# Kernel optimization log

Hardware: AMD Instinct MI355X
Metric: run time of the kernel (lower is better)

## Reference

```python
import jax, jax.numpy as jnp
import numpy as np

SCALE_FACTORS = (1, 2, 4)
N, T, F = 4096, 128, 128
MARKET = 64
MIX = sum(T // k for k in SCALE_FACTORS)  # 224


def hardswish(x):
    return x * jnp.clip(x + 3.0, 0.0, 6.0) * (1.0 / 6.0)


def layernorm2d(x, g, b, eps=1e-5):
    # LayerNorm with normalized_shape == last two dims (as in torch nn.LayerNorm((A, B)))
    mu = jnp.mean(x, axis=(-2, -1), keepdims=True)
    var = jnp.var(x, axis=(-2, -1), keepdims=True)
    return (x - mu) * jax.lax.rsqrt(var + eps) * g + b


def setup_inputs() -> dict:
    key = jax.random.key(0)
    ks = jax.random.split(key, 32)
    inp = {"x": jax.random.normal(ks[0], (N, T, F), jnp.float32)}
    i = 1
    for si, k in enumerate(SCALE_FACTORS):
        tk = T // k
        inp[f"cw{si}"] = jax.random.normal(ks[i], (F, F, k), jnp.float32) * 0.05; i += 1
        inp[f"cb{si}"] = jnp.zeros((F,), jnp.float32)
        inp[f"lg{si}"] = jnp.ones((tk, F), jnp.float32)
        inp[f"lb{si}"] = jnp.zeros((tk, F), jnp.float32)
        inp[f"L1_{si}"] = jax.random.normal(ks[i], (tk, tk), jnp.float32) * 0.01; i += 1
        inp[f"L2_{si}"] = jax.random.normal(ks[i], (tk, tk), jnp.float32) * 0.01; i += 1
    inp["fc_w"] = jax.random.normal(ks[i], (1, F), jnp.float32) * 0.05; i += 1
    inp["fc_b"] = jnp.zeros((1,), jnp.float32)
    inp["sm_lg"] = jnp.ones((N, MIX), jnp.float32)
    inp["sm_lb"] = jnp.zeros((N, MIX), jnp.float32)
    inp["M1"] = jax.random.normal(ks[i], (MARKET, N), jnp.float32); i += 1
    inp["M2"] = jax.random.normal(ks[i], (N, MARKET), jnp.float32); i += 1
    inp["sm_fc_w"] = jax.random.normal(ks[i], (1, 2 * MIX), jnp.float32) * 0.02; i += 1
    inp["sm_fc_b"] = jnp.zeros((1,), jnp.float32)
    return inp


def _forward(x, cw0, cb0, lg0, lb0, L1_0, L2_0,
             cw1, cb1, lg1, lb1, L1_1, L2_1,
             cw2, cb2, lg2, lb2, L1_2, L2_2,
             fc_w, fc_b, sm_lg, sm_lb, M1, M2, sm_fc_w, sm_fc_b):
    n, t, f = x.shape
    per_scale = ((cw0, cb0, lg0, lb0, L1_0, L2_0),
                 (cw1, cb1, lg1, lb1, L1_1, L2_1),
                 (cw2, cb2, lg2, lb2, L1_2, L2_2))
    parts = []
    for k, (cw, cb, lg, lb, L1, L2) in zip(SCALE_FACTORS, per_scale):
        tk = t // k
        # Conv1d(kernel=k, stride=k) == blockwise contraction over non-overlapping windows
        xr = x.transpose(0, 2, 1).reshape(n, f, tk, k)          # (n, F_in, tk, k)
        xt = jnp.einsum('nitk,oik->nto', xr, cw) + cb            # (n, tk, F)
        # TimeMixing: ragged prefix loop == single lower-triangular matmul over time
        mask = jnp.tril(jnp.ones((tk, tk), x.dtype))
        h = layernorm2d(xt, lg, lb)
        u = hardswish(jnp.einsum('ts,nsf->ntf', L1 * mask, h))
        v = jnp.einsum('ts,nsf->ntf', L2 * mask, u)
        xt = xt + v
        parts.append(xt @ fc_w[0] + fc_b[0])                     # (n, tk)
    h = jnp.concatenate(parts, axis=1)                           # (n, MIX)
    # StockMixing
    hn = layernorm2d(h, sm_lg, sm_lb)
    z = M2 @ hardswish(M1 @ hn)                                  # (n, MIX)
    out = jnp.concatenate([h, h + z], axis=1)                    # (n, 2*MIX)
    return out @ sm_fc_w[0][:, None] + sm_fc_b                   # (n, 1)


def reference(x, cw0, cb0, lg0, lb0, L1_0, L2_0,
              cw1, cb1, lg1, lb1, L1_1, L2_1,
              cw2, cb2, lg2, lb2, L1_2, L2_2,
              fc_w, fc_b, sm_lg, sm_lb, M1, M2, sm_fc_w, sm_fc_b):
    return _forward(x, cw0, cb0, lg0, lb0, L1_0, L2_0,
                    cw1, cb1, lg1, lb1, L1_1, L2_1,
                    cw2, cb2, lg2, lb2, L1_2, L2_2,
                    fc_w, fc_b, sm_lg, sm_lb, M1, M2, sm_fc_w, sm_fc_b)
```

## Files before the change

kernel.cpp:

```cpp
#include <hip/hip_runtime.h>
#include <stdint.h>

typedef __attribute__((ext_vector_type(8))) short short8;
typedef __attribute__((ext_vector_type(4))) float f32x4;
typedef __attribute__((ext_vector_type(4))) unsigned short us4;

__device__ __forceinline__ unsigned short f2bf(float f) {
  union { float f; unsigned int i; } v; v.f = f;
  return (unsigned short)((v.i + 0x7FFFu + ((v.i >> 16) & 1u)) >> 16);
}
__device__ __forceinline__ float hswish(float x) {
  float t = fminf(fmaxf(x + 3.f, 0.f), 6.f);
  return x * t * (1.f / 6.f);
}
__device__ __forceinline__ short8 ldcvt8(const float* __restrict__ p) {
  float4 v0 = *(const float4*)p;
  float4 v1 = *(const float4*)(p + 4);
  short8 r;
  r[0] = (short)f2bf(v0.x); r[1] = (short)f2bf(v0.y);
  r[2] = (short)f2bf(v0.z); r[3] = (short)f2bf(v0.w);
  r[4] = (short)f2bf(v1.x); r[5] = (short)f2bf(v1.y);
  r[6] = (short)f2bf(v1.z); r[7] = (short)f2bf(v1.w);
  return r;
}

__global__ void prep_kernel(const float* __restrict__ cw0, const float* __restrict__ cw1,
                            const float* __restrict__ cw2,
                            const float* __restrict__ L1_0, const float* __restrict__ L2_0,
                            const float* __restrict__ L1_1, const float* __restrict__ L2_1,
                            const float* __restrict__ L1_2, const float* __restrict__ L2_2,
                            unsigned short* __restrict__ ws16) {
  int idx = blockIdx.x * 256 + threadIdx.x;
  if (idx < 16384) {
    ws16[idx] = f2bf(cw0[idx]);
  } else if (idx < 49152) {
    int t = idx - 16384; int o = t >> 8, m = t & 255, j = m >> 7, i = m & 127;
    ws16[idx] = f2bf(cw1[(o * 128 + i) * 2 + j]);
  } else if (idx < 114688) {
    int t = idx - 49152; int o = t >> 9, m = t & 511, j = m >> 7, i = m & 127;
    ws16[idx] = f2bf(cw2[(o * 128 + i) * 4 + j]);
  } else if (idx < 212992) {
    int u = idx - 114688; int which = u >> 14; int e = u & 16383;
    int t = e >> 7, s = e & 127;
    float val = 0.f;
    if (which == 0)      { if (s <= t) val = L1_0[t * 128 + s]; }
    else if (which == 1) { if (s <= t) val = L2_0[t * 128 + s]; }
    else if (which == 2) { if ((s >> 6) == (t >> 6) && (s & 63) <= (t & 63)) val = L1_1[(t & 63) * 64 + (s & 63)]; }
    else if (which == 3) { if ((s >> 6) == (t >> 6) && (s & 63) <= (t & 63)) val = L2_1[(t & 63) * 64 + (s & 63)]; }
    else if (which == 4) { if ((s >> 5) == (t >> 5) && (s & 31) <= (t & 31)) val = L1_2[(t & 31) * 32 + (s & 31)]; }
    else                 { if ((s >> 5) == (t >> 5) && (s & 31) <= (t & 31)) val = L2_2[(t & 31) * 32 + (s & 31)]; }
    ws16[idx] = f2bf(val);
  }
}

__global__ void xcvt_kernel(const float* __restrict__ x, unsigned short* __restrict__ xbf) {
  const float4* x4 = (const float4*)x;
  us4* o4 = (us4*)xbf;
#pragma unroll
  for (int j = 0; j < 4; ++j) {
    int idx = blockIdx.x * 1024 + j * 256 + threadIdx.x;
    float4 v = x4[idx];
    us4 p; p[0] = f2bf(v.x); p[1] = f2bf(v.y); p[2] = f2bf(v.z); p[3] = f2bf(v.w);
    o4[idx] = p;
  }
}

template <bool XBF>
__device__ __forceinline__ short8 load_a(const float* __restrict__ xf,
                                         const unsigned short* __restrict__ xb, int off) {
  if constexpr (XBF) return *(const short8*)&xb[off];
  else return ldcvt8(xf + off);
}

template <int S, bool XBF>
__launch_bounds__(256, 3)
__global__ void s1_tile(const float* __restrict__ xf, const unsigned short* __restrict__ xb,
                        const float* __restrict__ cb, const float* __restrict__ lg,
                        const float* __restrict__ lb,
                        const float* __restrict__ fc_w, const float* __restrict__ fc_b,
                        const unsigned short* __restrict__ cwLT,
                        const unsigned short* __restrict__ L1blk,
                        const unsigned short* __restrict__ L2blk,
                        float* __restrict__ h_out) {
  constexpr int K = 128 << S;
  constexpr int LOG2TK = 7 - S;
  constexpr int TKM = (128 >> S) - 1;
  constexpr int SAMPLES = 1 << S;
  constexpr int OFF = (S == 0) ? 0 : (S == 1 ? 128 : 192);
  constexpr int NK = K / 32;
  constexpr int GSH = 3 - S;
  constexpr float INVD = 1.f / (float)((TKM + 1) * 128);

  __shared__ unsigned short HT[128 * 128];
  __shared__ float scr[272];
  float* part = scr + 128;

  const int tid = threadIdx.x, wave = tid >> 6, lane = tid & 63;
  const int quad = lane >> 4, l16 = lane & 15;
  const int Tb = (wave & 1) * 4, Ob = (wave >> 1) * 4;
  const int n0 = blockIdx.x << S;
  const int abase = n0 * 16384;
  const float fcb = fc_b[0];

  if (tid < 128) { scr[tid] = fc_w[tid]; part[tid] = 0.f; }
  else if (tid < 144) scr[tid + 128] = 0.f;
  __syncthreads();

  f32x4 acc[4][4];
#pragma unroll
  for (int tt = 0; tt < 4; ++tt)
#pragma unroll
    for (int oo = 0; oo < 4; ++oo) acc[tt][oo] = (f32x4){0.f, 0.f, 0.f, 0.f};
#pragma unroll
  for (int ks = 0; ks < NK; ++ks) {
    short8 a[4];
#pragma unroll
    for (int tt = 0; tt < 4; ++tt)
      a[tt] = load_a<XBF>(xf, xb, abase + ((Tb + tt) * 16 + l16) * K + ks * 32 + quad * 8);
#pragma unroll
    for (int oo = 0; oo < 4; ++oo) {
      short8 b = *(const short8*)&cwLT[((Ob + oo) * 16 + l16) * K + ks * 32 + quad * 8];
#pragma unroll
      for (int tt = 0; tt < 4; ++tt)
        acc[tt][oo] = __builtin_amdgcn_mfma_f32_16x16x32_bf16(a[tt], b, acc[tt][oo], 0, 0, 0);
    }
  }

  float ts[4] = {0.f, 0.f, 0.f, 0.f}, tq[4] = {0.f, 0.f, 0.f, 0.f};
#pragma unroll
  for (int oo = 0; oo < 4; ++oo) {
    float cbv = cb[(Ob + oo) * 16 + l16];
#pragma unroll
    for (int tt = 0; tt < 4; ++tt)
#pragma unroll
      for (int r = 0; r < 4; ++r) {
        float v = acc[tt][oo][r] + cbv;
        acc[tt][oo][r] = v;
        ts[tt] += v; tq[tt] += v * v;
      }
  }
  {
    constexpr int GPW = (S == 2) ? 2 : 1;
    float gs[2] = {0.f, 0.f}, gq[2] = {0.f, 0.f};
#pragma unroll
    for (int tt = 0; tt < 4; ++tt) {
      int gl = (S == 2) ? (tt >> 1) : 0;
      gs[gl] += ts[tt]; gq[gl] += tq[tt];
    }
#pragma unroll
    for (int j = 0; j < GPW; ++j) {
      float s = gs[j], q = gq[j];
#pragma unroll
      for (int m = 32; m >= 1; m >>= 1) { s += __shfl_xor(s, m); q += __shfl_xor(q, m); }
      if (lane == 0) {
        int g = (Tb >> GSH) + j;
        atomicAdd(&scr[256 + 2 * g], s);
        atomicAdd(&scr[257 + 2 * g], q);
      }
    }
  }
  __syncthreads();
  if (tid < SAMPLES) {
    float mu = scr[256 + 2 * tid] * INVD;
    float var = scr[257 + 2 * tid] * INVD - mu * mu;
    scr[264 + tid] = mu; scr[268 + tid] = rsqrtf(var + 1e-5f);
  }
  __syncthreads();

#pragma unroll
  for (int tt = 0; tt < 4; ++tt)
#pragma unroll
    for (int r = 0; r < 4; ++r) {
      float v = 0.f;
#pragma unroll
      for (int oo = 0; oo < 4; ++oo) v += acc[tt][oo][r] * scr[(Ob + oo) * 16 + l16];
      v += __shfl_xor(v, 1); v += __shfl_xor(v, 2);
      v += __shfl_xor(v, 4); v += __shfl_xor(v, 8);
      if (l16 == 0) atomicAdd(&part[(Tb + tt) * 16 + quad * 4 + r], v);
    }

#pragma unroll
  for (int tt = 0; tt < 4; ++tt) {
    int tile = Tb + tt, g = tile >> GSH;
    float mu = scr[264 + g], rs = scr[268 + g];
    int tlb = (tile * 16) & TKM;
#pragma unroll
    for (int oo = 0; oo < 4; ++oo) {
      int f = (Ob + oo) * 16 + l16;
      int kf = (f ^ (f >> 3)) & 15;
#pragma unroll
      for (int r = 0; r < 4; ++r) {
        int t = tile * 16 + quad * 4 + r;
        int tl = tlb + quad * 4 + r;
        float hv = (acc[tt][oo][r] - mu) * rs * lg[tl * 128 + f] + lb[tl * 128 + f];
        HT[f * 128 + ((((t >> 3) ^ kf) << 3) | (t & 7))] = f2bf(hv);
      }
    }
  }
  __syncthreads();

  f32x4 u[4][4];
#pragma unroll
  for (int tt = 0; tt < 4; ++tt)
#pragma unroll
    for (int oo = 0; oo < 4; ++oo) u[tt][oo] = (f32x4){0.f, 0.f, 0.f, 0.f};
#pragma unroll
  for (int ks = 0; ks < 4; ++ks) {
    short8 a[4]; bool act[4]; bool any = false;
#pragma unroll
    for (int tt = 0; tt < 4; ++tt) {
      int tile = Tb + tt, g = tile >> GSH;
      act[tt] = (ks * 32 <= tile * 16 + 15) && (ks * 32 + 31 >= (g << LOG2TK));
      if (act[tt]) { a[tt] = *(const short8*)&L1blk[(tile * 16 + l16) * 128 + ks * 32 + quad * 8]; any = true; }
    }
    if (!any) continue;
#pragma unroll
    for (int oo = 0; oo < 4; ++oo) {
      int f = (Ob + oo) * 16 + l16;
      int kf = (f ^ (f >> 3)) & 15;
      short8 b = *(const short8*)&HT[f * 128 + (((ks * 4 + quad) ^ kf) << 3)];
#pragma unroll
      for (int tt = 0; tt < 4; ++tt)
        if (act[tt]) u[tt][oo] = __builtin_amdgcn_mfma_f32_16x16x32_bf16(a[tt], b, u[tt][oo], 0, 0, 0);
    }
  }
  __syncthreads();

#pragma unroll
  for (int tt = 0; tt < 4; ++tt) {
    int tile = Tb + tt;
#pragma unroll
    for (int oo = 0; oo < 4; ++oo) {
      int f = (Ob + oo) * 16 + l16;
      int kf = (f ^ (f >> 3)) & 15;
#pragma unroll
      for (int r = 0; r < 4; ++r) {
        int t = tile * 16 + quad * 4 + r;
        HT[f * 128 + ((((t >> 3) ^ kf) << 3) | (t & 7))] = f2bf(hswish(u[tt][oo][r]));
      }
    }
  }
  __syncthreads();

#pragma unroll
  for (int tt = 0; tt < 4; ++tt)
#pragma unroll
    for (int oo = 0; oo < 4; ++oo) u[tt][oo] = (f32x4){0.f, 0.f, 0.f, 0.f};
#pragma unroll
  for (int ks = 0; ks < 4; ++ks) {
    short8 a[4]; bool act[4]; bool any = false;
#pragma unroll
    for (int tt = 0; tt < 4; ++tt) {
      int tile = Tb + tt, g = tile >> GSH;
      act[tt] = (ks * 32 <= tile * 16 + 15) && (ks * 32 + 31 >= (g << LOG2TK));
      if (act[tt]) { a[tt] = *(const short8*)&L2blk[(tile * 16 + l16) * 128 + ks * 32 + quad * 8]; any = true; }
    }
    if (!any) continue;
#pragma unroll
    for (int oo = 0; oo < 4; ++oo) {
      int f = (Ob + oo) * 16 + l16;
      int kf = (f ^ (f >> 3)) & 15;
      short8 b = *(const short8*)&HT[f * 128 + (((ks * 4 + quad) ^ kf) << 3)];
#pragma unroll
      for (int tt = 0; tt < 4; ++tt)
        if (act[tt]) u[tt][oo] = __builtin_amdgcn_mfma_f32_16x16x32_bf16(a[tt], b, u[tt][oo], 0, 0, 0);
    }
  }

#pragma unroll
  for (int tt = 0; tt < 4; ++tt)
#pragma unroll
    for (int r = 0; r < 4; ++r) {
      float v = 0.f;
#pragma unroll
      for (int oo = 0; oo < 4; ++oo) v += u[tt][oo][r] * scr[(Ob + oo) * 16 + l16];
      v += __shfl_xor(v, 1); v += __shfl_xor(v, 2);
      v += __shfl_xor(v, 4); v += __shfl_xor(v, 8);
      if (l16 == 0) atomicAdd(&part[(Tb + tt) * 16 + quad * 4 + r], v);
    }
  __syncthreads();

  if (tid < 128) {
    int g = tid >> LOG2TK, tl = tid & TKM;
    h_out[(size_t)(n0 + g) * 224 + OFF + tl] = part[tid] + fcb;
  }
}

__global__ void stats_kernel(const float* __restrict__ h, float* __restrict__ stats) {
  int base = blockIdx.x * 4096;
  float s = 0.f, ss = 0.f;
  for (int j = 0; j < 16; ++j) {
    float v = h[base + j * 256 + threadIdx.x];
    s += v; ss += v * v;
  }
  int lane = threadIdx.x & 63, wave = threadIdx.x >> 6;
#pragma unroll
  for (int m = 32; m >= 1; m >>= 1) { s += __shfl_xor(s, m); ss += __shfl_xor(ss, m); }
  __shared__ float red[8];
  if (lane == 0) { red[wave * 2] = s; red[wave * 2 + 1] = ss; }
  __syncthreads();
  if (threadIdx.x == 0) {
    atomicAdd(&stats[0], red[0] + red[2] + red[4] + red[6]);
    atomicAdd(&stats[1], red[1] + red[3] + red[5] + red[7]);
  }
}

__global__ void mix1_kernel(const float* __restrict__ h,
                            const float* __restrict__ sm_lg,
                            const float* __restrict__ sm_lb,
                            const float* __restrict__ M1,
                            const float* __restrict__ stats,
                            float* __restrict__ A) {
  const int m = blockIdx.x, seg = blockIdx.y;
  const int r = threadIdx.x & 63, ch = threadIdx.x >> 6;
  const float inv = 1.f / 917504.f;
  float mu = stats[0] * inv;
  float var = stats[1] * inv - mu * mu;
  float rsig = rsqrtf(var + 1e-5f);
  float acc = 0.f;
  int n0 = seg * 1024 + ch * 256;
  for (int i = 0; i < 256; ++i) {
    int n = n0 + i;
    float hn = (h[n * 224 + m] - mu) * rsig * sm_lg[n * 224 + m] + sm_lb[n * 224 + m];
    acc += M1[r * 4096 + n] * hn;
  }
  __shared__ float red[256];
  red[threadIdx.x] = acc;
  __syncthreads();
  if (threadIdx.x < 64)
    atomicAdd(&A[threadIdx.x * 224 + m],
              red[threadIdx.x] + red[64 + threadIdx.x] + red[128 + threadIdx.x] + red[192 + threadIdx.x]);
}

__global__ void mix2_kernel(const float* __restrict__ A,
                            const float* __restrict__ sm_fc_w,
                            float* __restrict__ cvec) {
  int r = threadIdx.x & 63, ch = threadIdx.x >> 6;
  float acc = 0.f;
  for (int j = ch; j < 224; j += 4)
    acc += hswish(A[r * 224 + j]) * sm_fc_w[224 + j];
  __shared__ float red[256];
  red[threadIdx.x] = acc;
  __syncthreads();
  if (threadIdx.x < 64)
    cvec[threadIdx.x] = red[threadIdx.x] + red[64 + threadIdx.x] + red[128 + threadIdx.x] + red[192 + threadIdx.x];
}

__global__ void out_kernel(const float* __restrict__ h,
                           const float* __restrict__ M2,
                           const float* __restrict__ cvec,
                           const float* __restrict__ sm_fc_w,
                           const float* __restrict__ sm_fc_b,
                           float* __restrict__ out) {
  int wave = threadIdx.x >> 6, lane = threadIdx.x & 63;
  int n = blockIdx.x * 4 + wave;
  float acc = M2[n * 64 + lane] * cvec[lane];
  for (int j = lane; j < 224; j += 64)
    acc += h[n * 224 + j] * (sm_fc_w[j] + sm_fc_w[224 + j]);
#pragma unroll
  for (int m = 32; m >= 1; m >>= 1) acc += __shfl_xor(acc, m);
  if (lane == 0) out[n] = acc + sm_fc_b[0];
}

extern "C" void kernel_launch(void* const* d_in, const int* in_sizes, int n_in,
                              void* d_out, int out_size, void* d_ws, size_t ws_size,
                              hipStream_t stream) {
  const float* x      = (const float*)d_in[0];
  const float* cw0    = (const float*)d_in[1];
  const float* cb0    = (const float*)d_in[2];
  const float* lg0    = (const float*)d_in[3];
  const float* lb0    = (const float*)d_in[4];
  const float* L1_0   = (const float*)d_in[5];
  const float* L2_0   = (const float*)d_in[6];
  const float* cw1    = (const float*)d_in[7];
  const float* cb1    = (const float*)d_in[8];
  const float* lg1    = (const float*)d_in[9];
  const float* lb1    = (const float*)d_in[10];
  const float* L1_1   = (const float*)d_in[11];
  const float* L2_1   = (const float*)d_in[12];
  const float* cw2    = (const float*)d_in[13];
  const float* cb2    = (const float*)d_in[14];
  const float* lg2    = (const float*)d_in[15];
  const float* lb2    = (const float*)d_in[16];
  const float* L1_2   = (const float*)d_in[17];
  const float* L2_2   = (const float*)d_in[18];
  const float* fc_w   = (const float*)d_in[19];
  const float* fc_b   = (const float*)d_in[20];
  const float* sm_lg  = (const float*)d_in[21];
  const float* sm_lb  = (const float*)d_in[22];
  const float* M1     = (const float*)d_in[23];
  const float* M2     = (const float*)d_in[24];
  const float* sm_fc_w = (const float*)d_in[25];
  const float* sm_fc_b = (const float*)d_in[26];

  char* ws = (char*)d_ws;
  unsigned short* ws16 = (unsigned short*)ws;
  float* h     = (float*)(ws + 425984);
  float* stats = (float*)(ws + 4096000);
  float* A     = (float*)(ws + 4096256);
  float* cvec  = (float*)(ws + 4153600);
  unsigned short* xbf = (unsigned short*)(ws + 4194304);
  const bool use_xbf = ws_size >= 138412032ULL;

  const unsigned short* cwLT0 = ws16;
  const unsigned short* cwLT1 = ws16 + 16384;
  const unsigned short* cwLT2 = ws16 + 49152;
  const unsigned short* L1b0 = ws16 + 114688;
  const unsigned short* L2b0 = ws16 + 131072;
  const unsigned short* L1b1 = ws16 + 147456;
  const unsigned short* L2b1 = ws16 + 163840;
  const unsigned short* L1b2 = ws16 + 180224;
  const unsigned short* L2b2 = ws16 + 196608;

  prep_kernel<<<832, 256, 0, stream>>>(cw0, cw1, cw2, L1_0, L2_0, L1_1, L2_1, L1_2, L2_2, ws16);

  if (use_xbf) {
    xcvt_kernel<<<16384, 256, 0, stream>>>(x, xbf);
    s1_tile<0, true><<<4096, 256, 0, stream>>>(x, xbf, cb0, lg0, lb0, fc_w, fc_b, cwLT0, L1b0, L2b0, h);
    s1_tile<1, true><<<2048, 256, 0, stream>>>(x, xbf, cb1, lg1, lb1, fc_w, fc_b, cwLT1, L1b1, L2b1, h);
    s1_tile<2, true><<<1024, 256, 0, stream>>>(x, xbf, cb2, lg2, lb2, fc_w, fc_b, cwLT2, L1b2, L2b2, h);
  } else {
    s1_tile<0, false><<<4096, 256, 0, stream>>>(x, xbf, cb0, lg0, lb0, fc_w, fc_b, cwLT0, L1b0, L2b0, h);
    s1_tile<1, false><<<2048, 256, 0, stream>>>(x, xbf, cb1, lg1, lb1, fc_w, fc_b, cwLT1, L1b1, L2b1, h);
    s1_tile<2, false><<<1024, 256, 0, stream>>>(x, xbf, cb2, lg2, lb2, fc_w, fc_b, cwLT2, L1b2, L2b2, h);
  }

  hipMemsetAsync(ws + 4096000, 0, 57600, stream);
  stats_kernel<<<224, 256, 0, stream>>>(h, stats);
  mix1_kernel<<<dim3(224, 4), 256, 0, stream>>>(h, sm_lg, sm_lb, M1, stats, A);
  mix2_kernel<<<1, 256, 0, stream>>>(A, sm_fc_w, cvec);
  out_kernel<<<1024, 256, 0, stream>>>(h, M2, cvec, sm_fc_w, sm_fc_b, (float*)d_out);
}
```

Measured before the change: 902.0 us.

## Merge per-scale tile kernels into one launch, fuse stats, pre-transpose operands

```diff
diff --git a/kernel.cpp b/kernel.cpp
--- a/kernel.cpp
+++ b/kernel.cpp
@@ -24,12 +24,37 @@
   return r;
 }
 
+#define WS16_OFF   0ULL
+#define M1T_OFF    425984ULL
+#define LGT0_OFF   1474560ULL
+#define LBT0_OFF   1540096ULL
+#define LGT1_OFF   1605632ULL
+#define LBT1_OFF   1638400ULL
+#define LGT2_OFF   1671168ULL
+#define LBT2_OFF   1687552ULL
+#define H_OFF      1703936ULL
+#define HT_OFF     5373952ULL
+#define STATS_OFF  9043968ULL
+#define A_OFF      9044224ULL
+#define CVEC_OFF   9101568ULL
+#define XBF_OFF    9437184ULL
+#define WS_NEED    143654912ULL
+
 __global__ void prep_kernel(const float* __restrict__ cw0, const float* __restrict__ cw1,
                             const float* __restrict__ cw2,
                             const float* __restrict__ L1_0, const float* __restrict__ L2_0,
                             const float* __restrict__ L1_1, const float* __restrict__ L2_1,
                             const float* __restrict__ L1_2, const float* __restrict__ L2_2,
-                            unsigned short* __restrict__ ws16) {
+                            const float* __restrict__ M1,
+                            const float* __restrict__ lg0, const float* __restrict__ lb0,
+                            const float* __restrict__ lg1, const float* __restrict__ lb1,
+                            const float* __restrict__ lg2, const float* __restrict__ lb2,
+                            char* __restrict__ ws) {
+  unsigned short* ws16 = (unsigned short*)(ws + WS16_OFF);
+  float* m1t  = (float*)(ws + M1T_OFF);
+  float* lgT0 = (float*)(ws + LGT0_OFF); float* lbT0 = (float*)(ws + LBT0_OFF);
+  float* lgT1 = (float*)(ws + LGT1_OFF); float* lbT1 = (float*)(ws + LBT1_OFF);
+  float* lgT2 = (float*)(ws + LGT2_OFF); float* lbT2 = (float*)(ws + LBT2_OFF);
   int idx = blockIdx.x * 256 + threadIdx.x;
   if (idx < 16384) {
     ws16[idx] = f2bf(cw0[idx]);
@@ -50,6 +75,21 @@
     else if (which == 4) { if ((s >> 5) == (t >> 5) && (s & 31) <= (t & 31)) val = L1_2[(t & 31) * 32 + (s & 31)]; }
     else                 { if ((s >> 5) == (t >> 5) && (s & 31) <= (t & 31)) val = L2_2[(t & 31) * 32 + (s & 31)]; }
     ws16[idx] = f2bf(val);
+  } else if (idx < 475136) {
+    int e = idx - 212992; int n = e >> 6, r = e & 63;
+    m1t[e] = M1[r * 4096 + n];
+  } else if (idx < 491520) {
+    int e = idx - 475136; int f = e >> 7, t = e & 127; lgT0[e] = lg0[t * 128 + f];
+  } else if (idx < 507904) {
+    int e = idx - 491520; int f = e >> 7, t = e & 127; lbT0[e] = lb0[t * 128 + f];
+  } else if (idx < 516096) {
+    int e = idx - 507904; int f = e >> 6, t = e & 63;  lgT1[e] = lg1[t * 128 + f];
+  } else if (idx < 524288) {
+    int e = idx - 516096; int f = e >> 6, t = e & 63;  lbT1[e] = lb1[t * 128 + f];
+  } else if (idx < 528384) {
+    int e = idx - 524288; int f = e >> 5, t = e & 31;  lgT2[e] = lg2[t * 128 + f];
+  } else if (idx < 532480) {
+    int e = idx - 528384; int f = e >> 5, t = e & 31;  lbT2[e] = lb2[t * 128 + f];
   }
 }
 
@@ -65,42 +105,32 @@
   }
 }
 
-template <bool XBF>
-__device__ __forceinline__ short8 load_a(const float* __restrict__ xf,
-                                         const unsigned short* __restrict__ xb, int off) {
-  if constexpr (XBF) return *(const short8*)&xb[off];
-  else return ldcvt8(xf + off);
-}
-
 template <int S, bool XBF>
-__launch_bounds__(256, 3)
-__global__ void s1_tile(const float* __restrict__ xf, const unsigned short* __restrict__ xb,
-                        const float* __restrict__ cb, const float* __restrict__ lg,
-                        const float* __restrict__ lb,
-                        const float* __restrict__ fc_w, const float* __restrict__ fc_b,
-                        const unsigned short* __restrict__ cwLT,
-                        const unsigned short* __restrict__ L1blk,
-                        const unsigned short* __restrict__ L2blk,
-                        float* __restrict__ h_out) {
+__device__ __forceinline__ void s1_body(
+    int bidx,
+    const float* __restrict__ xf, const unsigned short* __restrict__ xb,
+    const float* __restrict__ cb, const float* __restrict__ lgT, const float* __restrict__ lbT,
+    const float* __restrict__ fc_w, const float* __restrict__ fc_b,
+    const unsigned short* __restrict__ cwLT,
+    const unsigned short* __restrict__ L1blk, const unsigned short* __restrict__ L2blk,
+    float* __restrict__ h_out, float* __restrict__ hT, float* __restrict__ stats,
+    unsigned short* __restrict__ HT, float* __restrict__ scr) {
   constexpr int K = 128 << S;
   constexpr int LOG2TK = 7 - S;
   constexpr int TKM = (128 >> S) - 1;
+  constexpr int TK = 128 >> S;
   constexpr int SAMPLES = 1 << S;
   constexpr int OFF = (S == 0) ? 0 : (S == 1 ? 128 : 192);
   constexpr int NK = K / 32;
   constexpr int GSH = 3 - S;
-  constexpr float INVD = 1.f / (float)((TKM + 1) * 128);
-
-  __shared__ unsigned short HT[128 * 128];
-  __shared__ float scr[272];
+  constexpr float INVD = 1.f / (float)(TK * 128);
+
   float* part = scr + 128;
-
   const int tid = threadIdx.x, wave = tid >> 6, lane = tid & 63;
   const int quad = lane >> 4, l16 = lane & 15;
   const int Tb = (wave & 1) * 4, Ob = (wave >> 1) * 4;
-  const int n0 = blockIdx.x << S;
-  const int abase = n0 * 16384;
-  const float fcb = fc_b[0];
+  const int n0 = bidx << S;
+  const size_t xbase = (size_t)n0 * 16384;
 
   if (tid < 128) { scr[tid] = fc_w[tid]; part[tid] = 0.f; }
   else if (tid < 144) scr[tid + 128] = 0.f;
@@ -111,12 +141,15 @@
   for (int tt = 0; tt < 4; ++tt)
 #pragma unroll
     for (int oo = 0; oo < 4; ++oo) acc[tt][oo] = (f32x4){0.f, 0.f, 0.f, 0.f};
-#pragma unroll
+#pragma unroll 4
   for (int ks = 0; ks < NK; ++ks) {
     short8 a[4];
 #pragma unroll
-    for (int tt = 0; tt < 4; ++tt)
-      a[tt] = load_a<XBF>(xf, xb, abase + ((Tb + tt) * 16 + l16) * K + ks * 32 + quad * 8);
+    for (int tt = 0; tt < 4; ++tt) {
+      size_t off = xbase + (size_t)((Tb + tt) * 16 + l16) * K + ks * 32 + quad * 8;
+      if constexpr (XBF) a[tt] = *(const short8*)&xb[off];
+      else a[tt] = ldcvt8(xf + off);
+    }
 #pragma unroll
     for (int oo = 0; oo < 4; ++oo) {
       short8 b = *(const short8*)&cwLT[((Ob + oo) * 16 + l16) * K + ks * 32 + quad * 8];
@@ -183,16 +216,18 @@
   for (int tt = 0; tt < 4; ++tt) {
     int tile = Tb + tt, g = tile >> GSH;
     float mu = scr[264 + g], rs = scr[268 + g];
-    int tlb = (tile * 16) & TKM;
+    int tb = tile * 16 + quad * 4;
+    int tl = tb & TKM;
 #pragma unroll
     for (int oo = 0; oo < 4; ++oo) {
       int f = (Ob + oo) * 16 + l16;
       int kf = (f ^ (f >> 3)) & 15;
+      float4 lg4 = *(const float4*)&lgT[f * TK + tl];
+      float4 lb4 = *(const float4*)&lbT[f * TK + tl];
 #pragma unroll
       for (int r = 0; r < 4; ++r) {
-        int t = tile * 16 + quad * 4 + r;
-        int tl = tlb + quad * 4 + r;
-        float hv = (acc[tt][oo][r] - mu) * rs * lg[tl * 128 + f] + lb[tl * 128 + f];
+        int t = tb + r;
+        float hv = (acc[tt][oo][r] - mu) * rs * (&lg4.x)[r] + (&lb4.x)[r];
         HT[f * 128 + ((((t >> 3) ^ kf) << 3) | (t & 7))] = f2bf(hv);
       }
     }
@@ -229,13 +264,14 @@
 #pragma unroll
   for (int tt = 0; tt < 4; ++tt) {
     int tile = Tb + tt;
+    int tb = tile * 16 + quad * 4;
 #pragma unroll
     for (int oo = 0; oo < 4; ++oo) {
       int f = (Ob + oo) * 16 + l16;
       int kf = (f ^ (f >> 3)) & 15;
 #pragma unroll
       for (int r = 0; r < 4; ++r) {
-        int t = tile * 16 + quad * 4 + r;
+        int t = tb + r;
         HT[f * 128 + ((((t >> 3) ^ kf) << 3) | (t & 7))] = f2bf(hswish(u[tt][oo][r]));
       }
     }
@@ -281,48 +317,74 @@
   __syncthreads();
 
   if (tid < 128) {
+    float val = part[tid] + fc_b[0];
     int g = tid >> LOG2TK, tl = tid & TKM;
-    h_out[(size_t)(n0 + g) * 224 + OFF + tl] = part[tid] + fcb;
-  }
-}
-
-__global__ void stats_kernel(const float* __restrict__ h, float* __restrict__ stats) {
-  int base = blockIdx.x * 4096;
-  float s = 0.f, ss = 0.f;
-  for (int j = 0; j < 16; ++j) {
-    float v = h[base + j * 256 + threadIdx.x];
-    s += v; ss += v * v;
-  }
-  int lane = threadIdx.x & 63, wave = threadIdx.x >> 6;
-#pragma unroll
-  for (int m = 32; m >= 1; m >>= 1) { s += __shfl_xor(s, m); ss += __shfl_xor(ss, m); }
-  __shared__ float red[8];
-  if (lane == 0) { red[wave * 2] = s; red[wave * 2 + 1] = ss; }
-  __syncthreads();
-  if (threadIdx.x == 0) {
-    atomicAdd(&stats[0], red[0] + red[2] + red[4] + red[6]);
-    atomicAdd(&stats[1], red[1] + red[3] + red[5] + red[7]);
-  }
-}
-
-__global__ void mix1_kernel(const float* __restrict__ h,
+    int n = n0 + g;
+    h_out[(size_t)n * 224 + OFF + tl] = val;
+    hT[(size_t)(OFF + tl) * 4096 + n] = val;
+    float s = val, q = val * val;
+#pragma unroll
+    for (int m = 32; m >= 1; m >>= 1) { s += __shfl_xor(s, m); q += __shfl_xor(q, m); }
+    if (lane == 0) {
+      int slot = (int)(blockIdx.x & 31);
+      atomicAdd(&stats[2 * slot], s);
+      atomicAdd(&stats[2 * slot + 1], q);
+    }
+  }
+}
+
+template <bool XBF>
+__launch_bounds__(256, 4)
+__global__ void s1_all(const float* __restrict__ xf, const unsigned short* __restrict__ xb,
+                       const float* __restrict__ cb0, const float* __restrict__ cb1,
+                       const float* __restrict__ cb2,
+                       const float* __restrict__ fc_w, const float* __restrict__ fc_b,
+                       const char* __restrict__ wsc,
+                       float* __restrict__ h_out, float* __restrict__ hT,
+                       float* __restrict__ stats) {
+  __shared__ unsigned short HT[128 * 128];
+  __shared__ float scr[272];
+  const unsigned short* ws16 = (const unsigned short*)(wsc + WS16_OFF);
+  int b = blockIdx.x;
+  if (b < 1024) {
+    s1_body<2, XBF>(b, xf, xb, cb2,
+                    (const float*)(wsc + LGT2_OFF), (const float*)(wsc + LBT2_OFF),
+                    fc_w, fc_b, ws16 + 49152, ws16 + 180224, ws16 + 196608,
+                    h_out, hT, stats, HT, scr);
+  } else if (b < 3072) {
+    s1_body<1, XBF>(b - 1024, xf, xb, cb1,
+                    (const float*)(wsc + LGT1_OFF), (const float*)(wsc + LBT1_OFF),
+                    fc_w, fc_b, ws16 + 16384, ws16 + 147456, ws16 + 163840,
+                    h_out, hT, stats, HT, scr);
+  } else {
+    s1_body<0, XBF>(b - 3072, xf, xb, cb0,
+                    (const float*)(wsc + LGT0_OFF), (const float*)(wsc + LBT0_OFF),
+                    fc_w, fc_b, ws16, ws16 + 114688, ws16 + 131072,
+                    h_out, hT, stats, HT, scr);
+  }
+}
+
+__global__ void mix1_kernel(const float* __restrict__ hT,
                             const float* __restrict__ sm_lg,
                             const float* __restrict__ sm_lb,
-                            const float* __restrict__ M1,
+                            const float* __restrict__ m1t,
                             const float* __restrict__ stats,
                             float* __restrict__ A) {
-  const int m = blockIdx.x, seg = blockIdx.y;
-  const int r = threadIdx.x & 63, ch = threadIdx.x >> 6;
+  const int m = blockIdx.x;
+  const int seg = blockIdx.y;
+  const int r = threadIdx.x & 63, c = threadIdx.x >> 6;
+  float S = 0.f, Q = 0.f;
+#pragma unroll
+  for (int s = 0; s < 32; ++s) { S += stats[2 * s]; Q += stats[2 * s + 1]; }
   const float inv = 1.f / 917504.f;
-  float mu = stats[0] * inv;
-  float var = stats[1] * inv - mu * mu;
-  float rsig = rsqrtf(var + 1e-5f);
+  float mu = S * inv;
+  float rsig = rsqrtf(Q * inv - mu * mu + 1e-5f);
   float acc = 0.f;
-  int n0 = seg * 1024 + ch * 256;
-  for (int i = 0; i < 256; ++i) {
+  const int n0 = seg * 512 + c * 128;
+  for (int i = 0; i < 128; ++i) {
     int n = n0 + i;
-    float hn = (h[n * 224 + m] - mu) * rsig * sm_lg[n * 224 + m] + sm_lb[n * 224 + m];
-    acc += M1[r * 4096 + n] * hn;
+    float hn = (hT[m * 4096 + n] - mu) * rsig * sm_lg[n * 224 + m] + sm_lb[n * 224 + m];
+    acc += m1t[n * 64 + r] * hn;
   }
   __shared__ float red[256];
   red[threadIdx.x] = acc;
@@ -394,40 +456,27 @@
   const float* sm_fc_b = (const float*)d_in[26];
 
   char* ws = (char*)d_ws;
-  unsigned short* ws16 = (unsigned short*)ws;
-  float* h     = (float*)(ws + 425984);
-  float* stats = (float*)(ws + 4096000);
-  float* A     = (float*)(ws + 4096256);
-  float* cvec  = (float*)(ws + 4153600);
-  unsigned short* xbf = (unsigned short*)(ws + 4194304);
-  const bool use_xbf = ws_size >= 138412032ULL;
-
-  const unsigned short* cwLT0 = ws16;
-  const unsigned short* cwLT1 = ws16 + 16384;
-  const unsigned short* cwLT2 = ws16 + 49152;
-  const unsigned short* L1b0 = ws16 + 114688;
-  const unsigned short* L2b0 = ws16 + 131072;
-  const unsigned short* L1b1 = ws16 + 147456;
-  const unsigned short* L2b1 = ws16 + 163840;
-  const unsigned short* L1b2 = ws16 + 180224;
-  const unsigned short* L2b2 = ws16 + 196608;
-
-  prep_kernel<<<832, 256, 0, stream>>>(cw0, cw1, cw2, L1_0, L2_0, L1_1, L2_1, L1_2, L2_2, ws16);
+  float* m1t   = (float*)(ws + M1T_OFF);
+  float* h     = (float*)(ws + H_OFF);
+  float* hT    = (float*)(ws + HT_OFF);
+  float* stats = (float*)(ws + STATS_OFF);
+  float* A     = (float*)(ws + A_OFF);
+  float* cvec  = (float*)(ws + CVEC_OFF);
+  unsigned short* xbf = (unsigned short*)(ws + XBF_OFF);
+  const bool use_xbf = ws_size >= WS_NEED;
+
+  prep_kernel<<<2080, 256, 0, stream>>>(cw0, cw1, cw2, L1_0, L2_0, L1_1, L2_1, L1_2, L2_2,
+                                        M1, lg0, lb0, lg1, lb1, lg2, lb2, ws);
+  hipMemsetAsync(ws + STATS_OFF, 0, 256 + 57344, stream);
 
   if (use_xbf) {
     xcvt_kernel<<<16384, 256, 0, stream>>>(x, xbf);
-    s1_tile<0, true><<<4096, 256, 0, stream>>>(x, xbf, cb0, lg0, lb0, fc_w, fc_b, cwLT0, L1b0, L2b0, h);
-    s1_tile<1, true><<<2048, 256, 0, stream>>>(x, xbf, cb1, lg1, lb1, fc_w, fc_b, cwLT1, L1b1, L2b1, h);
-    s1_tile<2, true><<<1024, 256, 0, stream>>>(x, xbf, cb2, lg2, lb2, fc_w, fc_b, cwLT2, L1b2, L2b2, h);
+    s1_all<true><<<7168, 256, 0, stream>>>(x, xbf, cb0, cb1, cb2, fc_w, fc_b, ws, h, hT, stats);
   } else {
-    s1_tile<0, false><<<4096, 256, 0, stream>>>(x, xbf, cb0, lg0, lb0, fc_w, fc_b, cwLT0, L1b0, L2b0, h);
-    s1_tile<1, false><<<2048, 256, 0, stream>>>(x, xbf, cb1, lg1, lb1, fc_w, fc_b, cwLT1, L1b1, L2b1, h);
-    s1_tile<2, false><<<1024, 256, 0, stream>>>(x, xbf, cb2, lg2, lb2, fc_w, fc_b, cwLT2, L1b2, L2b2, h);
-  }
-
-  hipMemsetAsync(ws + 4096000, 0, 57600, stream);
-  stats_kernel<<<224, 256, 0, stream>>>(h, stats);
-  mix1_kernel<<<dim3(224, 4), 256, 0, stream>>>(h, sm_lg, sm_lb, M1, stats, A);
+    s1_all<false><<<7168, 256, 0, stream>>>(x, xbf, cb0, cb1, cb2, fc_w, fc_b, ws, h, hT, stats);
+  }
+
+  mix1_kernel<<<dim3(224, 8), 256, 0, stream>>>(hT, sm_lg, sm_lb, m1t, stats, A);
   mix2_kernel<<<1, 256, 0, stream>>>(A, sm_fc_w, cvec);
   out_kernel<<<1024, 256, 0, stream>>>(h, M2, cvec, sm_fc_w, sm_fc_b, (float*)d_out);
 }
```

Result: slower. 999.1 us (+10.8%).
